# Kernel optimization log

Measured on AMD Instinct MI355X. Metric: run time of the kernel, lower is better.

Reference implementation:

```python
import jax, jax.numpy as jnp
import numpy as np

HID, PROJ, ATTN = 512, 1024, 128
B, L = 4, 2048


def _apply_rope(x):
    # x: [B, L, 2, ATTN]; RoPE over sequence dim (axis=1)
    half = x.shape[-1] // 2
    inv_freq = jnp.power(10000.0, -jnp.arange(half, dtype=jnp.float32) / half)
    pos = jnp.arange(x.shape[1], dtype=x.dtype)
    sinusoid = pos[:, None] * inv_freq.astype(x.dtype)          # [L, half]
    sin = jnp.sin(sinusoid)[None, :, None, :]                   # [1, L, 1, half]
    cos = jnp.cos(sinusoid)[None, :, None, :]
    x1, x2 = jnp.split(x, 2, axis=-1)
    return jnp.concatenate([x1 * cos - x2 * sin, x2 * cos + x1 * sin], axis=-1)


def setup_inputs() -> dict:
    key = jax.random.key(0)
    ks = jax.random.split(key, 8)
    node = jax.random.normal(ks[0], (B, L, HID), dtype=jnp.float32)
    bias = jax.random.normal(ks[1], (B, L, L), dtype=jnp.float32)
    scaling = jnp.full((1,), ATTN ** -0.5, dtype=jnp.float32)
    w1 = jax.random.normal(ks[2], (HID, 2 * PROJ + ATTN), dtype=jnp.float32) * (HID ** -0.5)
    b1 = jnp.zeros((2 * PROJ + ATTN,), dtype=jnp.float32)
    ms_weight = jax.random.normal(ks[3], (2, ATTN), dtype=jnp.float32) * 0.02
    ms_bias = jnp.zeros((2, ATTN), dtype=jnp.float32)
    w2 = jax.random.normal(ks[4], (PROJ, HID), dtype=jnp.float32) * (PROJ ** -0.5)
    b2 = jnp.zeros((HID,), dtype=jnp.float32)
    return {"node": node, "bias": bias, "scaling": scaling, "w1": w1, "b1": b1,
            "ms_weight": ms_weight, "ms_bias": ms_bias, "w2": w2, "b2": b2}


def reference(node, bias, scaling, w1, b1, ms_weight, ms_bias, w2, b2):
    # gated projection + SiLU
    gva = jax.nn.silu(node @ w1 + b1)                           # [B, L, 2P+A]
    gates, values, base = jnp.split(gva, [PROJ, 2 * PROJ], axis=-1)
    # multi-headed scaling -> [B, L, 2, A], then RoPE, then split q/k
    qk = base[..., None, :] * ms_weight + ms_bias               # [B, L, 2, A]
    qk = _apply_rope(qk)
    q, k = qk[..., 0, :], qk[..., 1, :]                         # [B, L, A]
    logits = jnp.einsum('bid,bjd->bij', q * scaling, k) + bias  # [B, L, L]
    attn = jax.nn.softmax(logits, axis=-1)
    out = jnp.einsum('bij,bjd->bid', attn, values)              # [B, L, P]
    return (out * gates) @ w2 + b2                              # [B, L, HID]
```

## Files before the change

### kernel.cpp

```cpp
#include <hip/hip_runtime.h>
#include <math.h>

#define HIDN 512
#define PROJ 1024
#define ATTN 128
#define BATCH 4
#define SEQ 2048
#define N1 (2*PROJ+ATTN)
#define ROWS (BATCH*SEQ)

typedef __attribute__((ext_vector_type(4))) float f32x4;
typedef __attribute__((ext_vector_type(8))) short bf16x8;

__device__ __forceinline__ short f2bf(float x){
    unsigned u = __builtin_bit_cast(unsigned, x);
    unsigned rounding = 0x7fffu + ((u >> 16) & 1u);
    u += rounding;
    return (short)(u >> 16);
}
__device__ __forceinline__ float bf2f(short s){
    unsigned u = ((unsigned)(unsigned short)s) << 16;
    return __builtin_bit_cast(float, u);
}

__device__ __forceinline__ void gload16(const void* g, void* l){
    __builtin_amdgcn_global_load_lds((const __attribute__((address_space(1))) void*)g,
                                     (__attribute__((address_space(3))) void*)l,
                                     16, 0, 0);
}

template<int BK, class Epi>
__device__ __forceinline__ void gemm_bt_tile(const short* __restrict__ A, int lda,
                                             const short* __restrict__ BT, int ldb,
                                             int m0, int n0, int K, Epi epi)
{
    __shared__ __align__(16) short lA[2][128*BK];
    __shared__ __align__(16) short lB[2][128*BK];
    const int t = threadIdx.x;
    const int lane = t & 63;
    const int w = t >> 6;
    const int wr = (w >> 1) * 64, wc = (w & 1) * 64;
    const int half = lane >> 4, l16 = lane & 15;
    constexpr int SPT = BK/16;

    f32x4 acc[4][4];
    #pragma unroll
    for (int i=0;i<4;i++)
        #pragma unroll
        for (int j=0;j<4;j++)
            acc[i][j] = (f32x4){0.f,0.f,0.f,0.f};

    auto stage = [&](int buf, int k0){
        #pragma unroll
        for (int i = 0; i < SPT; i++) {
            int li = i*256 + t;
            int r = li / (BK/8), s = li % (BK/8);
            int ss = (BK==64) ? (s ^ (r & 7)) : (s ^ ((r >> 1) & 3));
            gload16(A + (size_t)(m0+r)*lda + k0 + ss*8, lA[buf] + li*8);
        }
        #pragma unroll
        for (int i = 0; i < SPT; i++) {
            int li = i*256 + t;
            int r = li / (BK/8), s = li % (BK/8);
            int ss = (BK==64) ? (s ^ (r & 7)) : (s ^ ((r >> 1) & 3));
            gload16(BT + (size_t)(n0+r)*ldb + k0 + ss*8, lB[buf] + li*8);
        }
    };

    stage(0, 0);
    __syncthreads();
    int cur = 0;
    for (int k0 = BK; k0 <= K; k0 += BK) {
        if (k0 < K) stage(cur^1, k0);
        #pragma unroll
        for (int kk = 0; kk < BK; kk += 32) {
            bf16x8 af[4], bfr[4];
            const int cs = (kk >> 3) + half;
            #pragma unroll
            for (int i=0;i<4;i++){
                int row = wr + i*16 + l16;
                int sl = (BK==64) ? (cs ^ (row & 7)) : (cs ^ ((row >> 1) & 3));
                af[i] = *(const bf16x8*)(lA[cur] + row*BK + sl*8);
            }
            #pragma unroll
            for (int j=0;j<4;j++){
                int row = wc + j*16 + l16;
                int sl = (BK==64) ? (cs ^ (row & 7)) : (cs ^ ((row >> 1) & 3));
                bfr[j] = *(const bf16x8*)(lB[cur] + row*BK + sl*8);
            }
            #pragma unroll
            for (int i=0;i<4;i++)
                #pragma unroll
                for (int j=0;j<4;j++)
                    acc[i][j] = __builtin_amdgcn_mfma_f32_16x16x32_bf16(af[i], bfr[j], acc[i][j], 0, 0, 0);
        }
        __syncthreads();
        cur ^= 1;
    }
    #pragma unroll
    for (int i=0;i<4;i++)
        #pragma unroll
        for (int j=0;j<4;j++)
            #pragma unroll
            for (int q=0;q<4;q++)
                epi(m0 + wr + i*16 + half*4 + q, n0 + wc + j*16 + l16, acc[i][j][q]);
}

template<class Epi>
__device__ __forceinline__ void gemm_bt_tile256(const short* __restrict__ A, int lda,
                                                const short* __restrict__ BT, int ldb,
                                                int m0, int n0, int K, Epi epi)
{
    constexpr int BK = 32;
    __shared__ __align__(16) short lA[2][256*BK];
    __shared__ __align__(16) short lB[2][128*BK];
    const int t = threadIdx.x;
    const int lane = t & 63;
    const int w = t >> 6;
    const int wr = (w >> 1) * 64;
    const int wc = (w & 1) * 64;
    const int half = lane >> 4, l16 = lane & 15;

    f32x4 acc[4][4];
    #pragma unroll
    for (int i=0;i<4;i++)
        #pragma unroll
        for (int j=0;j<4;j++)
            acc[i][j] = (f32x4){0.f,0.f,0.f,0.f};

    auto stage = [&](int buf, int k0){
        #pragma unroll
        for (int i = 0; i < 2; i++) {
            int li = i*512 + t;
            int r = li >> 2, s = li & 3;
            int ss = s ^ ((r >> 1) & 3);
            gload16(A + (size_t)(m0+r)*lda + k0 + ss*8, lA[buf] + li*8);
        }
        {
            int li = t;
            int r = li >> 2, s = li & 3;
            int ss = s ^ ((r >> 1) & 3);
            gload16(BT + (size_t)(n0+r)*ldb + k0 + ss*8, lB[buf] + li*8);
        }
    };

    stage(0, 0);
    __syncthreads();
    int cur = 0;
    for (int k0 = BK; k0 <= K; k0 += BK) {
        if (k0 < K) stage(cur^1, k0);
        {
            bf16x8 af[4], bfr[4];
            const int cs = half;
            #pragma unroll
            for (int i=0;i<4;i++){
                int row = wr + i*16 + l16;
                af[i] = *(const bf16x8*)(lA[cur] + row*BK + (cs ^ ((row >> 1) & 3))*8);
            }
            #pragma unroll
            for (int j=0;j<4;j++){
                int row = wc + j*16 + l16;
                bfr[j] = *(const bf16x8*)(lB[cur] + row*BK + (cs ^ ((row >> 1) & 3))*8);
            }
            #pragma unroll
            for (int i=0;i<4;i++)
                #pragma unroll
                for (int j=0;j<4;j++)
                    acc[i][j] = __builtin_amdgcn_mfma_f32_16x16x32_bf16(af[i], bfr[j], acc[i][j], 0, 0, 0);
        }
        __syncthreads();
        cur ^= 1;
    }
    #pragma unroll
    for (int i=0;i<4;i++)
        #pragma unroll
        for (int j=0;j<4;j++)
            #pragma unroll
            for (int q=0;q<4;q++)
                epi(m0 + wr + i*16 + half*4 + q, n0 + wc + j*16 + l16, acc[i][j][q]);
}

__global__ void k_cast_node(const float* __restrict__ in, short* __restrict__ out){
    int idx = blockIdx.x*256 + threadIdx.x;
    float4 v0 = ((const float4*)in)[idx*2];
    float4 v1 = ((const float4*)in)[idx*2+1];
    bf16x8 o;
    o[0]=f2bf(v0.x); o[1]=f2bf(v0.y); o[2]=f2bf(v0.z); o[3]=f2bf(v0.w);
    o[4]=f2bf(v1.x); o[5]=f2bf(v1.y); o[6]=f2bf(v1.z); o[7]=f2bf(v1.w);
    ((bf16x8*)out)[idx] = o;
}

__global__ void k_transpose_cast(const float* __restrict__ in, short* __restrict__ out,
                                 int R, int C){
    __shared__ short tile[64][65];
    int r0 = blockIdx.y*64, c0 = blockIdx.x*64;
    int t = threadIdx.x;
    #pragma unroll
    for (int i=0;i<16;i++){
        int lin = i*256 + t; int r = lin>>6, c = lin&63;
        tile[r][c] = f2bf(in[(size_t)(r0+r)*C + c0+c]);
    }
    __syncthreads();
    #pragma unroll
    for (int i=0;i<16;i++){
        int lin = i*256 + t; int c = lin>>6, r = lin&63;
        out[(size_t)(c0+c)*R + r0+r] = tile[r][c];
    }
}

__global__ void k_transpose_v(const short* __restrict__ values, short* __restrict__ VT){
    __shared__ short tile[64][66];
    int z = blockIdx.z;
    int c0 = blockIdx.x*64, r0 = blockIdx.y*64;
    int t = threadIdx.x;
    #pragma unroll
    for (int i=0;i<2;i++){
        int idx = i*256 + t;
        int r = idx >> 3, cg = idx & 7;
        bf16x8 v = *(const bf16x8*)(values + (size_t)(z*SEQ + r0+r)*PROJ + c0 + cg*8);
        #pragma unroll
        for (int k=0;k<8;k++) tile[r][cg*8+k] = v[k];
    }
    __syncthreads();
    #pragma unroll
    for (int i=0;i<2;i++){
        int idx = i*256 + t;
        int c = idx >> 3, rg = idx & 7;
        bf16x8 v;
        #pragma unroll
        for (int k=0;k<8;k++) v[k] = tile[rg*8+k][c];
        *(bf16x8*)(VT + ((size_t)z*PROJ + c0+c)*SEQ + r0 + rg*8) = v;
    }
}

__global__ __launch_bounds__(512) void k_mm1(const short* __restrict__ nodeb,
        const short* __restrict__ w1T, const float* __restrict__ b1,
        short* __restrict__ gates, short* __restrict__ values){
    int b = blockIdx.x;
    int wg = (b & 7) * 64 + (b >> 3);
    int n0 = (wg & 15) * 128;
    int m0 = (wg >> 4) * 256;
    short* dst = (n0 < PROJ) ? gates : values;
    const int coff = (n0 < PROJ) ? 0 : PROJ;
    gemm_bt_tile256(nodeb, HIDN, w1T, HIDN, m0, n0, HIDN,
        [=](int row, int col, float v){
            v += b1[col];
            v = v / (1.f + __expf(-v));
            dst[(size_t)row*PROJ + (col - coff)] = f2bf(v);
        });
}

__global__ __launch_bounds__(256) void k_mmbase(const short* __restrict__ nodeb,
        const short* __restrict__ w1T, const float* __restrict__ b1,
        short* __restrict__ baseb){
    int m0 = blockIdx.x * 128;
    const short* BT = w1T + (size_t)(2*PROJ)*HIDN;
    gemm_bt_tile<32>(nodeb, HIDN, BT, HIDN, m0, 0, HIDN,
        [=](int row, int col, float v){
            v += b1[2*PROJ + col];
            v = v / (1.f + __expf(-v));
            baseb[(size_t)row*ATTN + col] = f2bf(v);
        });
}

__global__ void k_rope2(const short* __restrict__ baseb, const float* __restrict__ msw,
                        const float* __restrict__ msb, const float* __restrict__ scaling,
                        short* __restrict__ qb, short* __restrict__ kb){
    int idx = blockIdx.x*256 + threadIdx.x;
    int d = idx & 63;
    int row = idx >> 6;
    int l = row & (SEQ-1);
    float inv = exp2f(-(float)d * (13.287712379549449f/64.f));
    float ang = (float)l * inv;
    float s = sinf(ang), c = cosf(ang);
    const short* bp = baseb + (size_t)row*ATTN;
    float b_lo = bf2f(bp[d]), b_hi = bf2f(bp[d+64]);
    float x1q = b_lo*msw[d]        + msb[d];
    float x2q = b_hi*msw[d+64]     + msb[d+64];
    float x1k = b_lo*msw[128+d]    + msb[128+d];
    float x2k = b_hi*msw[128+d+64] + msb[128+d+64];
    float sc = scaling[0];
    qb[(size_t)row*ATTN + d]    = f2bf((x1q*c - x2q*s)*sc);
    qb[(size_t)row*ATTN + d+64] = f2bf((x2q*c + x1q*s)*sc);
    kb[(size_t)row*ATTN + d]    = f2bf(x1k*c - x2k*s);
    kb[(size_t)row*ATTN + d+64] = f2bf(x2k*c + x1k*s);
}

__global__ __launch_bounds__(256) void k_qksm(
        const short* __restrict__ qg, const short* __restrict__ kg,
        const float* __restrict__ bias, short* __restrict__ P,
        float* __restrict__ lsum16)
{
    __shared__ __align__(16) short smem[32768];
    __shared__ float sl[2][128];

    const int b = blockIdx.x;
    const int wg = (b & 7) * 128 + (b >> 3);
    const int z  = wg >> 8;
    const int qt = (wg >> 4) & 15;
    const int kt = wg & 15;
    const int q0 = qt * 128, kv0 = kt * 128;

    const int t = threadIdx.x;
    const int lane = t & 63, w = t >> 6;
    const int wr = (w >> 1)*64, wc = (w & 1)*64;
    const int half = lane >> 4, l16 = lane & 15;

    const short* Kg = kg + ((size_t)z*SEQ + kv0)*ATTN;
    const short* Qg = qg + ((size_t)z*SEQ + q0)*ATTN;

    #pragma unroll
    for (int i = 0; i < 8; i++) {
        int li = i*256 + t;
        int r = li >> 4, s = li & 15;
        int ss = s ^ (r & 15);
        gload16(Kg + (size_t)r*ATTN + ss*8, smem + li*8);
        gload16(Qg + (size_t)r*ATTN + ss*8, smem + 16384 + li*8);
    }

    f32x4 acc[4][4];
    #pragma unroll
    for (int i=0;i<4;i++)
        #pragma unroll
        for (int j=0;j<4;j++)
            acc[i][j] = *(const f32x4*)(bias
                + ((size_t)z*SEQ + q0 + wc + j*16 + l16)*SEQ
                + kv0 + wr + i*16 + half*4);

    __syncthreads();

    #pragma unroll
    for (int kk = 0; kk < 128; kk += 32) {
        const int cs = (kk >> 3) + half;
        bf16x8 af[4], bfr[4];
        #pragma unroll
        for (int i=0;i<4;i++){
            int row = wr + i*16 + l16;
            af[i] = *(const bf16x8*)(smem + row*128 + (cs ^ (row & 15))*8);
        }
        #pragma unroll
        for (int j=0;j<4;j++){
            int row = wc + j*16 + l16;
            bfr[j] = *(const bf16x8*)(smem + 16384 + row*128 + (cs ^ (row & 15))*8);
        }
        #pragma unroll
        for (int i=0;i<4;i++)
            #pragma unroll
            for (int j=0;j<4;j++)
                acc[i][j] = __builtin_amdgcn_mfma_f32_16x16x32_bf16(af[i], bfr[j], acc[i][j], 0, 0, 0);
    }

    __syncthreads();

    short* pt = smem;
    float tsum[4];
    #pragma unroll
    for (int j=0;j<4;j++){
        int col = wc + j*16 + l16;
        float sj = 0.f;
        #pragma unroll
        for (int i=0;i<4;i++){
            float p0=__expf(acc[i][j][0]), p1=__expf(acc[i][j][1]);
            float p2=__expf(acc[i][j][2]), p3=__expf(acc[i][j][3]);
            sj += p0+p1+p2+p3;
            short4 pv; pv.x=f2bf(p0); pv.y=f2bf(p1); pv.z=f2bf(p2); pv.w=f2bf(p3);
            *(short4*)(pt + col*136 + wr + i*16 + half*4) = pv;
        }
        tsum[j] = sj;
    }
    #pragma unroll
    for (int j=0;j<4;j++){
        tsum[j] += __shfl_xor(tsum[j],16,64);
        tsum[j] += __shfl_xor(tsum[j],32,64);
    }
    if (half==0){
        #pragma unroll
        for (int j=0;j<4;j++) sl[wr>>6][wc + j*16 + l16] = tsum[j];
    }
    __syncthreads();

    short* Pp = P + ((size_t)z*SEQ + q0)*SEQ + kv0;
    #pragma unroll
    for (int i=0;i<8;i++){
        int idx = i*256 + t;
        int q = idx >> 4, g = idx & 15;
        *(bf16x8*)(Pp + (size_t)q*SEQ + g*8) = *(const bf16x8*)(pt + q*136 + g*8);
    }
    if (t < 128)
        lsum16[(size_t)kt*ROWS + (size_t)z*SEQ + q0 + t] = sl[0][t] + sl[1][t];
}

__global__ void k_combine(const float* __restrict__ lsum16, float* __restrict__ linv){
    int r = blockIdx.x*256 + threadIdx.x;
    float s = 0.f;
    #pragma unroll
    for (int kt=0; kt<16; kt++) s += lsum16[(size_t)kt*ROWS + r];
    linv[r] = 1.f/s;
}

__global__ __launch_bounds__(256) void k_pv2(const short* __restrict__ P,
        const short* __restrict__ VT, const short* __restrict__ gates,
        const float* __restrict__ linv, short* __restrict__ a2){
    int b = blockIdx.x;
    int wg = (b & 7) * 64 + (b >> 3);
    int xx = wg & 7, yy = (wg >> 3) & 15, z = wg >> 7;
    const short* A = P  + (size_t)z*SEQ*SEQ;
    const short* B = VT + (size_t)z*PROJ*SEQ;
    int n0 = xx*128, m0 = yy*128;
    gemm_bt_tile<64>(A, SEQ, B, SEQ, m0, n0, SEQ,
        [=](int r, int c, float v){
            size_t ri = (size_t)z*SEQ + r;
            size_t gi = ri*PROJ + c;
            a2[gi] = f2bf(v * linv[ri] * bf2f(gates[gi]));
        });
}

__global__ __launch_bounds__(256) void k_mm2(const short* __restrict__ a2,
        const short* __restrict__ w2T, const float* __restrict__ b2,
        float* __restrict__ out){
    int b = blockIdx.x;
    int wg = (b & 7) * 32 + (b >> 3);
    int n0 = (wg & 3)*128, m0 = (wg >> 2)*128;
    gemm_bt_tile<64>(a2, PROJ, w2T, PROJ, m0, n0, PROJ,
        [=](int r, int c, float v){
            out[(size_t)r*HIDN + c] = v + b2[c];
        });
}

extern "C" void kernel_launch(void* const* d_in, const int* in_sizes, int n_in,
                              void* d_out, int out_size, void* d_ws, size_t ws_size,
                              hipStream_t stream) {
    const float* node    = (const float*)d_in[0];
    const float* bias    = (const float*)d_in[1];
    const float* scaling = (const float*)d_in[2];
    const float* w1      = (const float*)d_in[3];
    const float* b1      = (const float*)d_in[4];
    const float* msw     = (const float*)d_in[5];
    const float* msb     = (const float*)d_in[6];
    const float* w2      = (const float*)d_in[7];
    const float* b2      = (const float*)d_in[8];
    float* out = (float*)d_out;

    char* p = (char*)d_ws;
    auto alloc = [&](size_t bytes){ char* r = p; p += (bytes + 255) & ~(size_t)255; return r; };
    short* nodeb  = (short*)alloc((size_t)ROWS*HIDN*2);
    short* w1T    = (short*)alloc((size_t)N1*HIDN*2);
    short* w2T    = (short*)alloc((size_t)HIDN*PROJ*2);
    short* gates  = (short*)alloc((size_t)ROWS*PROJ*2);
    short* values = (short*)alloc((size_t)ROWS*PROJ*2);
    short* VT     = (short*)alloc((size_t)BATCH*PROJ*SEQ*2);
    short* baseb  = (short*)alloc((size_t)ROWS*ATTN*2);
    short* qb     = (short*)alloc((size_t)ROWS*ATTN*2);
    short* kb     = (short*)alloc((size_t)ROWS*ATTN*2);
    short* Pbuf   = (short*)alloc((size_t)BATCH*SEQ*SEQ*2);
    float* lsum16 = (float*)alloc((size_t)16*ROWS*4);
    float* linv   = (float*)alloc((size_t)ROWS*4);
    short* a2buf  = (short*)alloc((size_t)ROWS*PROJ*2);

    k_cast_node<<<ROWS*HIDN/2048, 256, 0, stream>>>(node, nodeb);
    k_transpose_cast<<<dim3(N1/64, HIDN/64), 256, 0, stream>>>(w1, w1T, HIDN, N1);
    k_transpose_cast<<<dim3(HIDN/64, PROJ/64), 256, 0, stream>>>(w2, w2T, PROJ, HIDN);
    k_mm1<<<16*(ROWS/256), 512, 0, stream>>>(nodeb, w1T, b1, gates, values);
    k_mmbase<<<ROWS/128, 256, 0, stream>>>(nodeb, w1T, b1, baseb);
    k_transpose_v<<<dim3(PROJ/64, SEQ/64, BATCH), 256, 0, stream>>>(values, VT);
    k_rope2<<<ROWS*64/256, 256, 0, stream>>>(baseb, msw, msb, scaling, qb, kb);
    k_qksm<<<16*16*BATCH, 256, 0, stream>>>(qb, kb, bias, Pbuf, lsum16);
    k_combine<<<ROWS/256, 256, 0, stream>>>(lsum16, linv);
    k_pv2<<<(PROJ/128)*(SEQ/128)*BATCH, 256, 0, stream>>>(Pbuf, VT, gates, linv, a2buf);
    k_mm2<<<(HIDN/128)*(ROWS/128), 256, 0, stream>>>(a2buf, w2T, b2, out);
}
```

Before: 146.6 us.

## Replace double-buffered LDS staging with single-buffer load-sync-compute loop in GEMM tiles

Removes the ping-pong LDS buffers in both GEMM tile routines. Each K step now issues its global-to-LDS loads, synchronises, computes, and synchronises again. This halves LDS usage, which may allow more resident workgroups per CU. In exchange, the next tile's loads no longer overlap with the current tile's MFMA work, so memory latency is exposed every iteration.

Result: slower. 162.9 us (+11.1%).

```diff
diff --git a/kernel.cpp b/kernel.cpp
--- a/kernel.cpp
+++ b/kernel.cpp
@@ -34,8 +34,8 @@
                                              const short* __restrict__ BT, int ldb,
                                              int m0, int n0, int K, Epi epi)
 {
-    __shared__ __align__(16) short lA[2][128*BK];
-    __shared__ __align__(16) short lB[2][128*BK];
+    __shared__ __align__(16) short lA[128*BK];
+    __shared__ __align__(16) short lB[128*BK];
     const int t = threadIdx.x;
     const int lane = t & 63;
     const int w = t >> 6;
@@ -50,28 +50,22 @@
         for (int j=0;j<4;j++)
             acc[i][j] = (f32x4){0.f,0.f,0.f,0.f};
 
-    auto stage = [&](int buf, int k0){
+    for (int k0 = 0; k0 < K; k0 += BK) {
         #pragma unroll
         for (int i = 0; i < SPT; i++) {
             int li = i*256 + t;
             int r = li / (BK/8), s = li % (BK/8);
             int ss = (BK==64) ? (s ^ (r & 7)) : (s ^ ((r >> 1) & 3));
-            gload16(A + (size_t)(m0+r)*lda + k0 + ss*8, lA[buf] + li*8);
+            gload16(A + (size_t)(m0+r)*lda + k0 + ss*8, lA + li*8);
         }
         #pragma unroll
         for (int i = 0; i < SPT; i++) {
             int li = i*256 + t;
             int r = li / (BK/8), s = li % (BK/8);
             int ss = (BK==64) ? (s ^ (r & 7)) : (s ^ ((r >> 1) & 3));
-            gload16(BT + (size_t)(n0+r)*ldb + k0 + ss*8, lB[buf] + li*8);
-        }
-    };
-
-    stage(0, 0);
-    __syncthreads();
-    int cur = 0;
-    for (int k0 = BK; k0 <= K; k0 += BK) {
-        if (k0 < K) stage(cur^1, k0);
+            gload16(BT + (size_t)(n0+r)*ldb + k0 + ss*8, lB + li*8);
+        }
+        __syncthreads();
         #pragma unroll
         for (int kk = 0; kk < BK; kk += 32) {
             bf16x8 af[4], bfr[4];
@@ -80,13 +74,13 @@
             for (int i=0;i<4;i++){
                 int row = wr + i*16 + l16;
                 int sl = (BK==64) ? (cs ^ (row & 7)) : (cs ^ ((row >> 1) & 3));
-                af[i] = *(const bf16x8*)(lA[cur] + row*BK + sl*8);
+                af[i] = *(const bf16x8*)(lA + row*BK + sl*8);
             }
             #pragma unroll
             for (int j=0;j<4;j++){
                 int row = wc + j*16 + l16;
                 int sl = (BK==64) ? (cs ^ (row & 7)) : (cs ^ ((row >> 1) & 3));
-                bfr[j] = *(const bf16x8*)(lB[cur] + row*BK + sl*8);
+                bfr[j] = *(const bf16x8*)(lB + row*BK + sl*8);
             }
             #pragma unroll
             for (int i=0;i<4;i++)
@@ -95,7 +89,6 @@
                     acc[i][j] = __builtin_amdgcn_mfma_f32_16x16x32_bf16(af[i], bfr[j], acc[i][j], 0, 0, 0);
         }
         __syncthreads();
-        cur ^= 1;
     }
     #pragma unroll
     for (int i=0;i<4;i++)
@@ -112,8 +105,8 @@
                                                 int m0, int n0, int K, Epi epi)
 {
     constexpr int BK = 32;
-    __shared__ __align__(16) short lA[2][256*BK];
-    __shared__ __align__(16) short lB[2][128*BK];
+    __shared__ __align__(16) short lA[256*BK];
+    __shared__ __align__(16) short lB[128*BK];
     const int t = threadIdx.x;
     const int lane = t & 63;
     const int w = t >> 6;
@@ -128,39 +121,33 @@
         for (int j=0;j<4;j++)
             acc[i][j] = (f32x4){0.f,0.f,0.f,0.f};
 
-    auto stage = [&](int buf, int k0){
+    for (int k0 = 0; k0 < K; k0 += BK) {
         #pragma unroll
         for (int i = 0; i < 2; i++) {
             int li = i*512 + t;
             int r = li >> 2, s = li & 3;
             int ss = s ^ ((r >> 1) & 3);
-            gload16(A + (size_t)(m0+r)*lda + k0 + ss*8, lA[buf] + li*8);
+            gload16(A + (size_t)(m0+r)*lda + k0 + ss*8, lA + li*8);
         }
         {
             int li = t;
             int r = li >> 2, s = li & 3;
             int ss = s ^ ((r >> 1) & 3);
-            gload16(BT + (size_t)(n0+r)*ldb + k0 + ss*8, lB[buf] + li*8);
-        }
-    };
-
-    stage(0, 0);
-    __syncthreads();
-    int cur = 0;
-    for (int k0 = BK; k0 <= K; k0 += BK) {
-        if (k0 < K) stage(cur^1, k0);
+            gload16(BT + (size_t)(n0+r)*ldb + k0 + ss*8, lB + li*8);
+        }
+        __syncthreads();
         {
             bf16x8 af[4], bfr[4];
             const int cs = half;
             #pragma unroll
             for (int i=0;i<4;i++){
                 int row = wr + i*16 + l16;
-                af[i] = *(const bf16x8*)(lA[cur] + row*BK + (cs ^ ((row >> 1) & 3))*8);
+                af[i] = *(const bf16x8*)(lA + row*BK + (cs ^ ((row >> 1) & 3))*8);
             }
             #pragma unroll
             for (int j=0;j<4;j++){
                 int row = wc + j*16 + l16;
-                bfr[j] = *(const bf16x8*)(lB[cur] + row*BK + (cs ^ ((row >> 1) & 3))*8);
+                bfr[j] = *(const bf16x8*)(lB + row*BK + (cs ^ ((row >> 1) & 3))*8);
             }
             #pragma unroll
             for (int i=0;i<4;i++)
@@ -169,7 +156,6 @@
                     acc[i][j] = __builtin_amdgcn_mfma_f32_16x16x32_bf16(af[i], bfr[j], acc[i][j], 0, 0, 0);
         }
         __syncthreads();
-        cur ^= 1;
     }
     #pragma unroll
     for (int i=0;i<4;i++)
```
